# Kernel optimization log

Hardware: AMD Instinct MI355X
Metric: run time of the kernel (lower is better)

The kernel has to match this reference:

```python
import jax, jax.numpy as jnp
import numpy as np

N_ATOMS = 50000
N_PAIRS = 1000000
F = 64   # per-atom features
G = 16   # radial basis functions
V = 32   # vector features
H1 = 128
IN_F = F + V + 1 + V  # 129, non-first interaction module
OUT_F = F + 2


def setup_inputs() -> dict:
    key = jax.random.key(0)
    ks = jax.random.split(key, 12)
    return {
        "atomic_embedding": jax.random.normal(ks[0], (N_ATOMS, F), dtype=jnp.float32),
        "partial_charges": jax.random.normal(ks[1], (N_ATOMS, 1), dtype=jnp.float32),
        "gs": jax.random.uniform(ks[2], (N_PAIRS, G), dtype=jnp.float32),
        "gv": jax.random.normal(ks[3], (N_PAIRS, 3, G), dtype=jnp.float32),
        "agh": jax.random.normal(ks[4], (F, G, V), dtype=jnp.float32) * (1.0 / np.sqrt(G)),
        "W1": jax.random.normal(ks[5], (IN_F, H1), dtype=jnp.float32) * (1.0 / np.sqrt(IN_F)),
        "b1": jnp.zeros((H1,), dtype=jnp.float32),
        "W2": jax.random.normal(ks[6], (H1, H1), dtype=jnp.float32) * (1.0 / np.sqrt(H1)),
        "b2": jnp.zeros((H1,), dtype=jnp.float32),
        "W3": jax.random.normal(ks[7], (H1, OUT_F), dtype=jnp.float32) * (1.0 / np.sqrt(H1)),
        "b3": jnp.zeros((OUT_F,), dtype=jnp.float32),
        "pair_indices": jax.random.randint(ks[8], (2, N_PAIRS), 0, N_ATOMS, dtype=jnp.int64),
    }


def _interaction(atomic_embedding, partial_charges, gs, gv, agh,
                 W1, b1, W2, b2, W3, b3, idx_j):
    n_atoms = atomic_embedding.shape[0]
    v = agh.shape[-1]

    # --- embedding branch ---
    a_j = atomic_embedding[idx_j]                      # (P, F) gather
    # torch: (gs[:,:,None] * a_j[:,None,:]).sum(1) == gs.sum(1, keepdims) * a_j
    avf_s = jnp.einsum('pg,pf->pf', gs, a_j)           # (P, F)
    radial_emb = jax.ops.segment_sum(avf_s, idx_j, num_segments=n_atoms)  # (N, F)

    avf_v = jnp.einsum('pa,pdg,agh->phd', a_j, gv, agh)  # (P, V, 3)
    vec_emb = jax.ops.segment_sum(jnp.sum(avf_v * avf_v, axis=-1),
                                  idx_j, num_segments=n_atoms)            # (N, V)

    # --- partial-charge branch (agh=None path) ---
    q_j = partial_charges[idx_j]                       # (P, 1)
    avf_s_q = jnp.einsum('pg,pf->pf', gs, q_j)         # (P, 1)
    radial_q = jax.ops.segment_sum(avf_s_q, idx_j, num_segments=n_atoms)  # (N, 1)
    vec_q = jnp.zeros((n_atoms, v), dtype=atomic_embedding.dtype)         # (N, V)

    msg = jnp.concatenate([radial_emb, vec_emb, radial_q, vec_q], axis=1)  # (N, F+V+1+V)

    h = jax.nn.gelu(msg @ W1 + b1, approximate=False)
    h = jax.nn.gelu(h @ W2 + b2, approximate=False)
    out = h @ W3 + b3                                   # (N, F+2)

    delta_q = out[:, 0:1]
    f = out[:, 1:2]
    delta_a = out[:, 2:]
    return delta_a, delta_q, f


def reference(atomic_embedding, partial_charges, gs, gv, agh,
              W1, b1, W2, b2, W3, b3, pair_indices):
    idx_j = pair_indices[1]
    return _interaction(atomic_embedding, partial_charges, gs, gv, agh,
                        W1, b1, W2, b2, W3, b3, idx_j)
```

## Files before the change

kernel.cpp:

```cpp
#include <hip/hip_runtime.h>
#include <math.h>

#define NA 50000
#define NP 1000000
#define OUTF 66
#define SCAN_BLOCKS 196


__global__ void k_hist(const int* __restrict__ idxj, int* __restrict__ cnt) {
    int p = blockIdx.x * 256 + threadIdx.x;
    if (p < NP) atomicAdd(&cnt[idxj[p]], 1);
}

__global__ __launch_bounds__(256) void k_scanA(const int* __restrict__ cnt,
                                               int* __restrict__ blkS) {
    __shared__ int sh[256];
    int t = threadIdx.x;
    int i = blockIdx.x * 256 + t;
    sh[t] = (i < NA) ? cnt[i] : 0;
    __syncthreads();
    for (int d = 128; d > 0; d >>= 1) {
        if (t < d) sh[t] += sh[t + d];
        __syncthreads();
    }
    if (t == 0) blkS[blockIdx.x] = sh[0];
}

__global__ __launch_bounds__(256) void k_scanB(int* __restrict__ blkS) {
    __shared__ int sh[256];
    int t = threadIdx.x;
    sh[t] = (t < SCAN_BLOCKS) ? blkS[t] : 0;
    __syncthreads();
    for (int d = 1; d < 256; d <<= 1) {
        int x = (t >= d) ? sh[t - d] : 0;
        __syncthreads();
        sh[t] += x;
        __syncthreads();
    }
    int e = (t == 0) ? 0 : sh[t - 1];
    if (t < SCAN_BLOCKS) blkS[t] = e;
}

__global__ __launch_bounds__(256) void k_scanC(const int* __restrict__ cnt,
                                               const int* __restrict__ blkS,
                                               int* __restrict__ offs,
                                               int* __restrict__ curs) {
    __shared__ int sh[256];
    int t = threadIdx.x;
    int i = blockIdx.x * 256 + t;
    sh[t] = (i < NA) ? cnt[i] : 0;
    __syncthreads();
    for (int d = 1; d < 256; d <<= 1) {
        int x = (t >= d) ? sh[t - d] : 0;
        __syncthreads();
        sh[t] += x;
        __syncthreads();
    }
    int excl = ((t == 0) ? 0 : sh[t - 1]) + blkS[blockIdx.x];
    if (i < NA) { offs[i] = excl; curs[i] = excl; }
}

__global__ void k_scatter(const int* __restrict__ idxj, int* __restrict__ curs,
                          int* __restrict__ sortedP) {
    int p = blockIdx.x * 256 + threadIdx.x;
    if (p < NP) {
        int i = idxj[p];
        int pos = atomicAdd(&curs[i], 1);
        sortedP[pos] = p;
    }
}

__global__ __launch_bounds__(256) void k_atoms(const float* __restrict__ emb,
                                               const float* __restrict__ agh,
                                               const float* __restrict__ gs,
                                               const float* __restrict__ gv,
                                               const int* __restrict__ sortedP,
                                               const int* __restrict__ offs,
                                               const int* __restrict__ cnt,
                                               float* __restrict__ S,
                                               float* __restrict__ vec) {
    __shared__ float embS[8][64];
    __shared__ float T_lds[8][32][20];
    const int t = threadIdx.x;
    const int atom0 = blockIdx.x * 8;

    for (int k = t; k < 8 * 64; k += 256)
        embS[k >> 6][k & 63] = emb[(size_t)(atom0 + (k >> 6)) * 64 + (k & 63)];
    __syncthreads();

    {
        float acc0[8], acc1[8];
#pragma unroll
        for (int at = 0; at < 8; ++at) { acc0[at] = 0.f; acc1[at] = 0.f; }
        const int gh0 = t, gh1 = t + 256;
        for (int a = 0; a < 64; ++a) {
            float w0 = agh[a * 512 + gh0];
            float w1 = agh[a * 512 + gh1];
#pragma unroll
            for (int at = 0; at < 8; ++at) {
                float e = embS[at][a];
                acc0[at] += e * w0;
                acc1[at] += e * w1;
            }
        }
        const int g0 = gh0 >> 5, h0 = gh0 & 31;
        const int g1 = gh1 >> 5, h1 = gh1 & 31;
#pragma unroll
        for (int at = 0; at < 8; ++at) {
            T_lds[at][h0][g0] = acc0[at];
            T_lds[at][h1][g1] = acc1[at];
        }
    }
    __syncthreads();

    const int wv = t >> 6, lane = t & 63;
    const int slot = lane >> 5, h = lane & 31;

    for (int at = 2 * wv; at < 2 * wv + 2; ++at) {
        const int i = atom0 + at;
        const int start = offs[i];
        const int n = cnt[i];

        float Tr[16];
#pragma unroll
        for (int g = 0; g < 16; ++g) Tr[g] = T_lds[at][h][g];

        float vacc = 0.f, gacc = 0.f;
        for (int it = 0; it < n; it += 2) {
            const int pi = it + slot;
            const bool ok = pi < n;
            if (ok) {
                const int p = sortedP[start + pi];
                float gr[48];
                const float4* gv4 = (const float4*)(gv + (size_t)p * 48);
#pragma unroll
                for (int q4 = 0; q4 < 12; ++q4) ((float4*)gr)[q4] = gv4[q4];

                float v0 = 0.f, v1 = 0.f, v2 = 0.f;
#pragma unroll
                for (int g = 0; g < 16; ++g) {
                    float tg = Tr[g];
                    v0 += gr[g] * tg;
                    v1 += gr[16 + g] * tg;
                    v2 += gr[32 + g] * tg;
                }
                vacc += v0 * v0 + v1 * v1 + v2 * v2;

                const float4* gs4 = (const float4*)(gs + (size_t)p * 16);
                float4 ga = gs4[0], gb = gs4[1], gc = gs4[2], gd = gs4[3];
                gacc += (ga.x + ga.y + ga.z + ga.w) + (gb.x + gb.y + gb.z + gb.w) +
                        (gc.x + gc.y + gc.z + gc.w) + (gd.x + gd.y + gd.z + gd.w);
            }
        }
        float vtot = vacc + __shfl_xor(vacc, 32);
        float gtot = gacc + __shfl_xor(gacc, 32);
        if (lane < 32) vec[(size_t)i * 32 + h] = vtot;
        if (lane == 0) S[i] = gtot;
    }
}

__global__ __launch_bounds__(256) void k_mlp(const float* __restrict__ emb,
                                             const float* __restrict__ q,
                                             const float* __restrict__ S,
                                             const float* __restrict__ vec,
                                             const float* __restrict__ W1,
                                             const float* __restrict__ b1,
                                             const float* __restrict__ W2,
                                             const float* __restrict__ b2,
                                             const float* __restrict__ W3,
                                             const float* __restrict__ b3,
                                             float* __restrict__ out) {
    __shared__ float msgS[32][97];
    __shared__ float h1S[32][128];
    __shared__ float h2S[32][128];
    const int t = threadIdx.x;
    const int atom0 = blockIdx.x * 32;

    for (int k = t; k < 32 * 97; k += 256) {
        int at = k / 97, c = k % 97;
        int i = atom0 + at;
        float val = 0.f;
        if (i < NA) {
            float s = S[i];
            if (c < 64) val = emb[(size_t)i * 64 + c] * s;
            else if (c < 96) val = vec[(size_t)i * 32 + (c - 64)];
            else val = q[i] * s;
        }
        msgS[at][c] = val;
    }
    __syncthreads();

    const int j = t & 127;
    const int base = (t >> 7) * 16;
    float acc[16];

#pragma unroll
    for (int r = 0; r < 16; ++r) acc[r] = b1[j];
    for (int k = 0; k < 97; ++k) {
        float w = W1[k * 128 + j];
#pragma unroll
        for (int r = 0; r < 16; ++r) acc[r] += msgS[base + r][k] * w;
    }
#pragma unroll
    for (int r = 0; r < 16; ++r) {
        float x = acc[r];
        h1S[base + r][j] = 0.5f * x * (1.f + erff(x * 0.70710678118654752f));
    }
    __syncthreads();

#pragma unroll
    for (int r = 0; r < 16; ++r) acc[r] = b2[j];
    for (int k = 0; k < 128; ++k) {
        float w = W2[k * 128 + j];
#pragma unroll
        for (int r = 0; r < 16; ++r) acc[r] += h1S[base + r][k] * w;
    }
#pragma unroll
    for (int r = 0; r < 16; ++r) {
        float x = acc[r];
        h2S[base + r][j] = 0.5f * x * (1.f + erff(x * 0.70710678118654752f));
    }
    __syncthreads();

    if (j < OUTF) {
#pragma unroll
        for (int r = 0; r < 16; ++r) acc[r] = b3[j];
        for (int k = 0; k < 128; ++k) {
            float w = W3[k * OUTF + j];
#pragma unroll
            for (int r = 0; r < 16; ++r) acc[r] += h2S[base + r][k] * w;
        }
#pragma unroll
        for (int r = 0; r < 16; ++r) {
            int i = atom0 + base + r;
            if (i < NA) {
                if (j == 0)
                    out[(size_t)NA * 64 + i] = acc[r];
                else if (j == 1)
                    out[(size_t)NA * 64 + NA + i] = acc[r];
                else
                    out[(size_t)i * 64 + (j - 2)] = acc[r];
            }
        }
    }
}

extern "C" void kernel_launch(void* const* d_in, const int* in_sizes, int n_in,
                              void* d_out, int out_size, void* d_ws, size_t ws_size,
                              hipStream_t stream) {
    const float* emb = (const float*)d_in[0];
    const float* q   = (const float*)d_in[1];
    const float* gs  = (const float*)d_in[2];
    const float* gv  = (const float*)d_in[3];
    const float* agh = (const float*)d_in[4];
    const float* W1  = (const float*)d_in[5];
    const float* b1  = (const float*)d_in[6];
    const float* W2  = (const float*)d_in[7];
    const float* b2  = (const float*)d_in[8];
    const float* W3  = (const float*)d_in[9];
    const float* b3  = (const float*)d_in[10];
    const int* pairs = (const int*)d_in[11];
    const int* idxj  = pairs + NP;

    int*   cnt     = (int*)d_ws;
    int*   offs    = cnt + NA;
    int*   curs    = offs + NA;
    int*   blkS    = curs + NA;
    int*   sortedP = blkS + 256;
    float* S       = (float*)(sortedP + NP);
    float* vec     = S + NA;

    hipMemsetAsync(cnt, 0, NA * sizeof(int), stream);
    k_hist<<<(NP + 255) / 256, 256, 0, stream>>>(idxj, cnt);
    k_scanA<<<SCAN_BLOCKS, 256, 0, stream>>>(cnt, blkS);
    k_scanB<<<1, 256, 0, stream>>>(blkS);
    k_scanC<<<SCAN_BLOCKS, 256, 0, stream>>>(cnt, blkS, offs, curs);
    k_scatter<<<(NP + 255) / 256, 256, 0, stream>>>(idxj, curs, sortedP);
    k_atoms<<<NA / 8, 256, 0, stream>>>(emb, agh, gs, gv, sortedP, offs, cnt, S, vec);
    k_mlp<<<(NA + 31) / 32, 256, 0, stream>>>(emb, q, S, vec,
                                              W1, b1, W2, b2, W3, b3,
                                              (float*)d_out);
}
```

Measured before the change: 929.8 us.

## Flatten per-block pair work in atom kernel and register-tile MLP

The atom kernel now handles all pairs of its 8 atoms as one flat range, packing the atom's low index bits into the sorted pair index. Each 4-lane group then handles one pair and accumulates into shared-memory atomics, which removes per-atom load imbalance and half-idle waves when pair counts vary. The MLP kernel moves to 64 atoms per block with an 8x4 register tile and float4 weight and activation loads, to raise arithmetic intensity. The costs are LDS atomic contention and a packed index that limits p to 2^28.

```diff
diff --git a/kernel.cpp b/kernel.cpp
--- a/kernel.cpp
+++ b/kernel.cpp
@@ -66,7 +66,7 @@
     if (p < NP) {
         int i = idxj[p];
         int pos = atomicAdd(&curs[i], 1);
-        sortedP[pos] = p;
+        sortedP[pos] = (p << 3) | (i & 7);
     }
 }
 
@@ -76,16 +76,19 @@
                                                const float* __restrict__ gv,
                                                const int* __restrict__ sortedP,
                                                const int* __restrict__ offs,
-                                               const int* __restrict__ cnt,
                                                float* __restrict__ S,
                                                float* __restrict__ vec) {
     __shared__ float embS[8][64];
     __shared__ float T_lds[8][32][20];
+    __shared__ float vecS[8][32];
+    __shared__ float sS[8];
     const int t = threadIdx.x;
     const int atom0 = blockIdx.x * 8;
 
+    vecS[t >> 5][t & 31] = 0.f;
+    if (t < 8) sS[t] = 0.f;
     for (int k = t; k < 8 * 64; k += 256)
-        embS[k >> 6][k & 63] = emb[(size_t)(atom0 + (k >> 6)) * 64 + (k & 63)];
+        embS[k >> 6][k & 63] = emb[(size_t)atom0 * 64 + k];
     __syncthreads();
 
     {
@@ -114,51 +117,57 @@
     __syncthreads();
 
     const int wv = t >> 6, lane = t & 63;
-    const int slot = lane >> 5, h = lane & 31;
-
-    for (int at = 2 * wv; at < 2 * wv + 2; ++at) {
-        const int i = atom0 + at;
-        const int start = offs[i];
-        const int n = cnt[i];
-
-        float Tr[16];
-#pragma unroll
-        for (int g = 0; g < 16; ++g) Tr[g] = T_lds[at][h][g];
-
-        float vacc = 0.f, gacc = 0.f;
-        for (int it = 0; it < n; it += 2) {
-            const int pi = it + slot;
-            const bool ok = pi < n;
-            if (ok) {
-                const int p = sortedP[start + pi];
-                float gr[48];
-                const float4* gv4 = (const float4*)(gv + (size_t)p * 48);
-#pragma unroll
-                for (int q4 = 0; q4 < 12; ++q4) ((float4*)gr)[q4] = gv4[q4];
-
+    const int pr = lane >> 2, q = lane & 3;
+    const int hb = q * 8;
+    const int start = offs[atom0];
+    const int end = (atom0 + 8 < NA) ? offs[atom0 + 8] : NP;
+
+    for (int k0 = start + wv * 16; k0 < end; k0 += 64) {
+        const int k = k0 + pr;
+        const bool ok = k < end;
+        int pk = ok ? sortedP[k] : 0;
+        const int p = pk >> 3, at = pk & 7;
+
+        float gq = 0.f;
+        if (ok) {
+            float4 g4 = ((const float4*)gs)[(size_t)p * 4 + q];
+            gq = (g4.x + g4.y) + (g4.z + g4.w);
+        }
+        gq += __shfl_xor(gq, 1);
+        gq += __shfl_xor(gq, 2);
+        if (ok && q == 0) atomicAdd(&sS[at], gq);
+
+        if (ok) {
+            float gvr[48];
+            const float4* gv4 = (const float4*)(gv + (size_t)p * 48);
+#pragma unroll
+            for (int j = 0; j < 12; ++j) ((float4*)gvr)[j] = gv4[j];
+
+#pragma unroll
+            for (int hh = 0; hh < 8; ++hh) {
+                const float4* Tr = (const float4*)&T_lds[at][hb + hh][0];
+                float4 t0 = Tr[0], t1 = Tr[1], t2 = Tr[2], t3 = Tr[3];
+                float Trow[16] = {t0.x, t0.y, t0.z, t0.w, t1.x, t1.y, t1.z, t1.w,
+                                  t2.x, t2.y, t2.z, t2.w, t3.x, t3.y, t3.z, t3.w};
                 float v0 = 0.f, v1 = 0.f, v2 = 0.f;
 #pragma unroll
                 for (int g = 0; g < 16; ++g) {
-                    float tg = Tr[g];
-                    v0 += gr[g] * tg;
-                    v1 += gr[16 + g] * tg;
-                    v2 += gr[32 + g] * tg;
+                    float tg = Trow[g];
+                    v0 += gvr[g] * tg;
+                    v1 += gvr[16 + g] * tg;
+                    v2 += gvr[32 + g] * tg;
                 }
-                vacc += v0 * v0 + v1 * v1 + v2 * v2;
-
-                const float4* gs4 = (const float4*)(gs + (size_t)p * 16);
-                float4 ga = gs4[0], gb = gs4[1], gc = gs4[2], gd = gs4[3];
-                gacc += (ga.x + ga.y + ga.z + ga.w) + (gb.x + gb.y + gb.z + gb.w) +
-                        (gc.x + gc.y + gc.z + gc.w) + (gd.x + gd.y + gd.z + gd.w);
-            }
-        }
-        float vtot = vacc + __shfl_xor(vacc, 32);
-        float gtot = gacc + __shfl_xor(gacc, 32);
-        if (lane < 32) vec[(size_t)i * 32 + h] = vtot;
-        if (lane == 0) S[i] = gtot;
-    }
-}
-
+                atomicAdd(&vecS[at][hb + hh], v0 * v0 + v1 * v1 + v2 * v2);
+            }
+        }
+    }
+    __syncthreads();
+
+    vec[(size_t)(atom0 + (t >> 5)) * 32 + (t & 31)] = vecS[t >> 5][t & 31];
+    if (t < 8) S[atom0 + t] = sS[t];
+}
+
+#define MSTR 132
 __global__ __launch_bounds__(256) void k_mlp(const float* __restrict__ emb,
                                              const float* __restrict__ q,
                                              const float* __restrict__ S,
@@ -170,15 +179,14 @@
                                              const float* __restrict__ W3,
                                              const float* __restrict__ b3,
                                              float* __restrict__ out) {
-    __shared__ float msgS[32][97];
-    __shared__ float h1S[32][128];
-    __shared__ float h2S[32][128];
+    __shared__ float bufA[64 * MSTR];
+    __shared__ float bufB[64 * MSTR];
     const int t = threadIdx.x;
-    const int atom0 = blockIdx.x * 32;
-
-    for (int k = t; k < 32 * 97; k += 256) {
-        int at = k / 97, c = k % 97;
-        int i = atom0 + at;
+    const int atom0 = blockIdx.x * 64;
+
+    for (int k = t; k < 64 * 97; k += 256) {
+        int a = k / 97, c = k - a * 97;
+        int i = atom0 + a;
         float val = 0.f;
         if (i < NA) {
             float s = S[i];
@@ -186,60 +194,124 @@
             else if (c < 96) val = vec[(size_t)i * 32 + (c - 64)];
             else val = q[i] * s;
         }
-        msgS[at][c] = val;
-    }
-    __syncthreads();
-
-    const int j = t & 127;
-    const int base = (t >> 7) * 16;
-    float acc[16];
-
-#pragma unroll
-    for (int r = 0; r < 16; ++r) acc[r] = b1[j];
-    for (int k = 0; k < 97; ++k) {
-        float w = W1[k * 128 + j];
-#pragma unroll
-        for (int r = 0; r < 16; ++r) acc[r] += msgS[base + r][k] * w;
-    }
-#pragma unroll
-    for (int r = 0; r < 16; ++r) {
-        float x = acc[r];
-        h1S[base + r][j] = 0.5f * x * (1.f + erff(x * 0.70710678118654752f));
-    }
-    __syncthreads();
-
-#pragma unroll
-    for (int r = 0; r < 16; ++r) acc[r] = b2[j];
-    for (int k = 0; k < 128; ++k) {
-        float w = W2[k * 128 + j];
-#pragma unroll
-        for (int r = 0; r < 16; ++r) acc[r] += h1S[base + r][k] * w;
-    }
-#pragma unroll
-    for (int r = 0; r < 16; ++r) {
-        float x = acc[r];
-        h2S[base + r][j] = 0.5f * x * (1.f + erff(x * 0.70710678118654752f));
-    }
-    __syncthreads();
-
-    if (j < OUTF) {
-#pragma unroll
-        for (int r = 0; r < 16; ++r) acc[r] = b3[j];
+        bufA[a * MSTR + c] = val;
+    }
+    __syncthreads();
+
+    const int jg = t & 31, ag = t >> 5;
+    const int j0 = 4 * jg;
+    const int abase = ag * 8;
+    float acc[8][4];
+
+    {
+        float4 bb = *(const float4*)&b1[j0];
+#pragma unroll
+        for (int a = 0; a < 8; ++a) {
+            acc[a][0] = bb.x; acc[a][1] = bb.y; acc[a][2] = bb.z; acc[a][3] = bb.w;
+        }
+        for (int k4 = 0; k4 < 96; k4 += 4) {
+            float4 w0 = *(const float4*)&W1[(k4 + 0) * 128 + j0];
+            float4 w1 = *(const float4*)&W1[(k4 + 1) * 128 + j0];
+            float4 w2 = *(const float4*)&W1[(k4 + 2) * 128 + j0];
+            float4 w3 = *(const float4*)&W1[(k4 + 3) * 128 + j0];
+#pragma unroll
+            for (int a = 0; a < 8; ++a) {
+                float4 m = *(const float4*)&bufA[(abase + a) * MSTR + k4];
+                acc[a][0] += m.x * w0.x + m.y * w1.x + m.z * w2.x + m.w * w3.x;
+                acc[a][1] += m.x * w0.y + m.y * w1.y + m.z * w2.y + m.w * w3.y;
+                acc[a][2] += m.x * w0.z + m.y * w1.z + m.z * w2.z + m.w * w3.z;
+                acc[a][3] += m.x * w0.w + m.y * w1.w + m.z * w2.w + m.w * w3.w;
+            }
+        }
+        {
+            float4 w = *(const float4*)&W1[96 * 128 + j0];
+#pragma unroll
+            for (int a = 0; a < 8; ++a) {
+                float m = bufA[(abase + a) * MSTR + 96];
+                acc[a][0] += m * w.x; acc[a][1] += m * w.y;
+                acc[a][2] += m * w.z; acc[a][3] += m * w.w;
+            }
+        }
+#pragma unroll
+        for (int a = 0; a < 8; ++a) {
+            float4 o;
+            o.x = 0.5f * acc[a][0] * (1.f + erff(acc[a][0] * 0.70710678118654752f));
+            o.y = 0.5f * acc[a][1] * (1.f + erff(acc[a][1] * 0.70710678118654752f));
+            o.z = 0.5f * acc[a][2] * (1.f + erff(acc[a][2] * 0.70710678118654752f));
+            o.w = 0.5f * acc[a][3] * (1.f + erff(acc[a][3] * 0.70710678118654752f));
+            *(float4*)&bufB[(abase + a) * MSTR + j0] = o;
+        }
+    }
+    __syncthreads();
+
+    {
+        float4 bb = *(const float4*)&b2[j0];
+#pragma unroll
+        for (int a = 0; a < 8; ++a) {
+            acc[a][0] = bb.x; acc[a][1] = bb.y; acc[a][2] = bb.z; acc[a][3] = bb.w;
+        }
+        for (int k4 = 0; k4 < 128; k4 += 4) {
+            float4 w0 = *(const float4*)&W2[(k4 + 0) * 128 + j0];
+            float4 w1 = *(const float4*)&W2[(k4 + 1) * 128 + j0];
+            float4 w2 = *(const float4*)&W2[(k4 + 2) * 128 + j0];
+            float4 w3 = *(const float4*)&W2[(k4 + 3) * 128 + j0];
+#pragma unroll
+            for (int a = 0; a < 8; ++a) {
+                float4 m = *(const float4*)&bufB[(abase + a) * MSTR + k4];
+                acc[a][0] += m.x * w0.x + m.y * w1.x + m.z * w2.x + m.w * w3.x;
+                acc[a][1] += m.x * w0.y + m.y * w1.y + m.z * w2.y + m.w * w3.y;
+                acc[a][2] += m.x * w0.z + m.y * w1.z + m.z * w2.z + m.w * w3.z;
+                acc[a][3] += m.x * w0.w + m.y * w1.w + m.z * w2.w + m.w * w3.w;
+            }
+        }
+#pragma unroll
+        for (int a = 0; a < 8; ++a) {
+            float4 o;
+            o.x = 0.5f * acc[a][0] * (1.f + erff(acc[a][0] * 0.70710678118654752f));
+            o.y = 0.5f * acc[a][1] * (1.f + erff(acc[a][1] * 0.70710678118654752f));
+            o.z = 0.5f * acc[a][2] * (1.f + erff(acc[a][2] * 0.70710678118654752f));
+            o.w = 0.5f * acc[a][3] * (1.f + erff(acc[a][3] * 0.70710678118654752f));
+            *(float4*)&bufA[(abase + a) * MSTR + j0] = o;
+        }
+    }
+    __syncthreads();
+
+    if (j0 < OUTF) {
+#pragma unroll
+        for (int a = 0; a < 8; ++a) {
+            acc[a][0] = b3[j0];
+            acc[a][1] = (j0 + 1 < OUTF) ? b3[j0 + 1] : 0.f;
+            acc[a][2] = (j0 + 2 < OUTF) ? b3[j0 + 2] : 0.f;
+            acc[a][3] = (j0 + 3 < OUTF) ? b3[j0 + 3] : 0.f;
+        }
         for (int k = 0; k < 128; ++k) {
-            float w = W3[k * OUTF + j];
-#pragma unroll
-            for (int r = 0; r < 16; ++r) acc[r] += h2S[base + r][k] * w;
-        }
-#pragma unroll
-        for (int r = 0; r < 16; ++r) {
-            int i = atom0 + base + r;
+            float w0 = W3[k * OUTF + j0];
+            float w1 = (j0 + 1 < OUTF) ? W3[k * OUTF + j0 + 1] : 0.f;
+            float w2 = (j0 + 2 < OUTF) ? W3[k * OUTF + j0 + 2] : 0.f;
+            float w3 = (j0 + 3 < OUTF) ? W3[k * OUTF + j0 + 3] : 0.f;
+#pragma unroll
+            for (int a = 0; a < 8; ++a) {
+                float m = bufA[(abase + a) * MSTR + k];
+                acc[a][0] += m * w0; acc[a][1] += m * w1;
+                acc[a][2] += m * w2; acc[a][3] += m * w3;
+            }
+        }
+#pragma unroll
+        for (int a = 0; a < 8; ++a) {
+            int i = atom0 + abase + a;
             if (i < NA) {
-                if (j == 0)
-                    out[(size_t)NA * 64 + i] = acc[r];
-                else if (j == 1)
-                    out[(size_t)NA * 64 + NA + i] = acc[r];
-                else
-                    out[(size_t)i * 64 + (j - 2)] = acc[r];
+#pragma unroll
+                for (int c = 0; c < 4; ++c) {
+                    int j = j0 + c;
+                    if (j < OUTF) {
+                        if (j == 0)
+                            out[(size_t)NA * 64 + i] = acc[a][c];
+                        else if (j == 1)
+                            out[(size_t)NA * 64 + NA + i] = acc[a][c];
+                        else
+                            out[(size_t)i * 64 + (j - 2)] = acc[a][c];
+                    }
+                }
             }
         }
     }
@@ -276,8 +348,8 @@
     k_scanB<<<1, 256, 0, stream>>>(blkS);
     k_scanC<<<SCAN_BLOCKS, 256, 0, stream>>>(cnt, blkS, offs, curs);
     k_scatter<<<(NP + 255) / 256, 256, 0, stream>>>(idxj, curs, sortedP);
-    k_atoms<<<NA / 8, 256, 0, stream>>>(emb, agh, gs, gv, sortedP, offs, cnt, S, vec);
-    k_mlp<<<(NA + 31) / 32, 256, 0, stream>>>(emb, q, S, vec,
+    k_atoms<<<NA / 8, 256, 0, stream>>>(emb, agh, gs, gv, sortedP, offs, S, vec);
+    k_mlp<<<(NA + 63) / 64, 256, 0, stream>>>(emb, q, S, vec,
                                               W1, b1, W2, b2, W3, b3,
                                               (float*)d_out);
 }
```

After: 806.1 us. -13.3%, faster.
